# Kernel tuning notes

Hardware: AMD Instinct MI355X
Metric: run time of the kernel (lower is better)

The kernel has to match this reference:

```python
import jax, jax.numpy as jnp
import numpy as np

D = 256
H = 8
FFN = 2048
EPS = 1e-5


def _layer_norm(x, g, b):
    m = jnp.mean(x, axis=-1, keepdims=True)
    v = jnp.mean((x - m) ** 2, axis=-1, keepdims=True)
    return (x - m) * jax.lax.rsqrt(v + EPS) * g + b


def _mha(q_in, k_in, v_in, wq, bq, wk, bk, wv, bv, wo, bo, mask):
    B, Sq, _ = q_in.shape
    Sk = k_in.shape[1]
    dh = D // H
    q = (q_in @ wq + bq).reshape(B, Sq, H, dh)
    k = (k_in @ wk + bk).reshape(B, Sk, H, dh)
    v = (v_in @ wv + bv).reshape(B, Sk, H, dh)
    scores = jnp.einsum('bqhd,bkhd->bhqk', q, k) / jnp.sqrt(jnp.float32(dh)).astype(q.dtype)
    if mask is not None:
        scores = scores + mask
    probs = jax.nn.softmax(scores, axis=-1)
    ctx = jnp.einsum('bhqk,bkhd->bqhd', probs, v).reshape(B, Sq, D)
    return ctx @ wo + bo


def setup_inputs() -> dict:
    key = jax.random.key(0)
    ks = jax.random.split(key, 32)
    s = 0.02
    def lin(i, din, dout):
        return jax.random.normal(ks[i], (din, dout), jnp.float32) * s
    inp = {
        'vision_encoder_hidden_states': jax.random.normal(ks[0], (4, 2048, D), jnp.float32),
        'text_encoder_hidden_states': jax.random.normal(ks[1], (4, 1024, D), jnp.float32),
        'vision_encoder_attention_mask': jnp.zeros((4, 1, 1, 2048), jnp.float32),
        'text_encoder_attention_mask': jnp.zeros((4, 1, 1, 1024), jnp.float32),
        'sa_wq': lin(2, D, D), 'sa_bq': jnp.zeros((D,), jnp.float32),
        'sa_wk': lin(3, D, D), 'sa_bk': jnp.zeros((D,), jnp.float32),
        'sa_wv': lin(4, D, D), 'sa_bv': jnp.zeros((D,), jnp.float32),
        'sa_wo': lin(5, D, D), 'sa_bo': jnp.zeros((D,), jnp.float32),
        'ca_wq': lin(6, D, D), 'ca_bq': jnp.zeros((D,), jnp.float32),
        'ca_wk': lin(7, D, D), 'ca_bk': jnp.zeros((D,), jnp.float32),
        'ca_wv': lin(8, D, D), 'ca_bv': jnp.zeros((D,), jnp.float32),
        'ca_wo': lin(9, D, D), 'ca_bo': jnp.zeros((D,), jnp.float32),
        'ln1_g': jnp.ones((D,), jnp.float32), 'ln1_b': jnp.zeros((D,), jnp.float32),
        'ln2_g': jnp.ones((D,), jnp.float32), 'ln2_b': jnp.zeros((D,), jnp.float32),
        'ln3_g': jnp.ones((D,), jnp.float32), 'ln3_b': jnp.zeros((D,), jnp.float32),
        'ln4_g': jnp.ones((D,), jnp.float32), 'ln4_b': jnp.zeros((D,), jnp.float32),
        'fc1_w': lin(10, D, FFN), 'fc1_b': jnp.zeros((FFN,), jnp.float32),
        'fc2_w': lin(11, FFN, D), 'fc2_b': jnp.zeros((D,), jnp.float32),
    }
    return inp


def reference(vision_encoder_hidden_states, text_encoder_hidden_states,
              vision_encoder_attention_mask, text_encoder_attention_mask,
              sa_wq, sa_bq, sa_wk, sa_bk, sa_wv, sa_bv, sa_wo, sa_bo,
              ca_wq, ca_bq, ca_wk, ca_bk, ca_wv, ca_bv, ca_wo, ca_bo,
              ln1_g, ln1_b, ln2_g, ln2_b, ln3_g, ln3_b, ln4_g, ln4_b,
              fc1_w, fc1_b, fc2_w, fc2_b):
    # self-attention over vision queries (dropout = identity in eval)
    residual = vision_encoder_hidden_states
    h = _mha(vision_encoder_hidden_states, vision_encoder_hidden_states,
             vision_encoder_hidden_states,
             sa_wq, sa_bq, sa_wk, sa_bk, sa_wv, sa_bv, sa_wo, sa_bo,
             vision_encoder_attention_mask)
    h = _layer_norm(residual + h, ln1_g, ln1_b)
    # text cross-attention
    res2 = h
    h = _mha(h, text_encoder_hidden_states, text_encoder_hidden_states,
             ca_wq, ca_bq, ca_wk, ca_bk, ca_wv, ca_bv, ca_wo, ca_bo,
             text_encoder_attention_mask)
    h = _layer_norm(res2 + h, ln2_g, ln2_b)
    # third block: residual + dropout(h) -> in eval this is h + h = 2h, then LN
    h = _layer_norm(h + h, ln3_g, ln3_b)
    # FFN
    res = h
    h = jax.nn.relu(h @ fc1_w + fc1_b)
    h = h @ fc2_w + fc2_b
    h = _layer_norm(res + h, ln4_g, ln4_b)
    return h
```

## Files before the change

### kernel.cpp

```cpp
#include <hip/hip_runtime.h>
#include <stdint.h>
#include <stddef.h>

#define HEADS 8
#define DH 32
#define DMODEL 256
#define LN_EPS 1e-5f
#define LOG2E 1.4426950408889634f
#define QSCALE 0.17677669529663687f
#define QSCALE2 (QSCALE * LOG2E)
#define EXP2(x) __builtin_amdgcn_exp2f(x)

typedef unsigned short u16;
typedef __bf16 bf16x8 __attribute__((ext_vector_type(8)));
typedef unsigned short u16x8 __attribute__((ext_vector_type(8)));
typedef float f32x4 __attribute__((ext_vector_type(4)));

static __device__ __forceinline__ u16 bfc(float f) {
    return __builtin_bit_cast(u16, (__bf16)f);
}
static __device__ __forceinline__ bf16x8 ldbf8(const u16* p) {
    return __builtin_bit_cast(bf16x8, *reinterpret_cast<const u16x8*>(p));
}
static __device__ __forceinline__ bf16x8 cvt8(float4 a, float4 b) {
    bf16x8 r;
    r[0] = (__bf16)a.x; r[1] = (__bf16)a.y; r[2] = (__bf16)a.z; r[3] = (__bf16)a.w;
    r[4] = (__bf16)b.x; r[5] = (__bf16)b.y; r[6] = (__bf16)b.z; r[7] = (__bf16)b.w;
    return r;
}

__global__ __launch_bounds__(256) void scale_mask(const float* __restrict__ in,
                                                  float* __restrict__ out, int n) {
    int i = blockIdx.x * 256 + threadIdx.x;
    if (i < n) out[i] = in[i] * LOG2E;
}

struct TDesc { const float* src; u16* dst; int K; int N; };
struct TArgs { TDesc d[10]; };

__global__ __launch_bounds__(256) void transpose_cvt(TArgs args) {
    TDesc d = args.d[blockIdx.y];
    const int ntx = d.N >> 5;
    const int tiles = (d.K >> 5) * ntx;
    if ((int)blockIdx.x >= tiles) return;
    const int tk = (blockIdx.x / ntx) << 5;
    const int tn = (blockIdx.x % ntx) << 5;
    __shared__ float t[32][33];
    const int lx = threadIdx.x & 31;
    const int ly = threadIdx.x >> 5;
#pragma unroll
    for (int i = 0; i < 4; ++i)
        t[ly + 8 * i][lx] = d.src[(size_t)(tk + ly + 8 * i) * d.N + tn + lx];
    __syncthreads();
#pragma unroll
    for (int i = 0; i < 4; ++i)
        d.dst[(size_t)(tn + ly + 8 * i) * d.K + tk + lx] = bfc(t[lx][ly + 8 * i]);
}

struct Slice { u16* out; const float* bias; int mode; float sc; };

__global__ __launch_bounds__(256) void gemm_xproj(
    const float* __restrict__ Af, const u16* __restrict__ Wt,
    Slice s0, Slice s1, Slice s2, int M, int ntm)
{
    const int lane = threadIdx.x & 63;
    const int wave = threadIdx.x >> 6;
    const int l15 = lane & 15, lhi = lane >> 4;
    const int tm = ((int)blockIdx.x % ntm) * 128;
    const int tn = ((int)blockIdx.x / ntm) * 64;
    const int wm = tm + wave * 32;
    const int sel = tn >> 8;
    const int tl = tn & 255;
    Slice sl = (sel == 0) ? s0 : (sel == 1 ? s1 : s2);

    const f32x4 z4 = {0.f, 0.f, 0.f, 0.f};
    f32x4 acc[2][4];
#pragma unroll
    for (int i = 0; i < 2; ++i)
#pragma unroll
        for (int j = 0; j < 4; ++j) acc[i][j] = z4;

    const float* ar0 = Af + (size_t)(wm + l15) * 256 + lhi * 8;
    const float* ar1 = ar0 + (size_t)16 * 256;
    const u16* b0p = Wt + (size_t)(tn + l15) * 256 + lhi * 8;

    float4 a00 = *(const float4*)(ar0), a01 = *(const float4*)(ar0 + 4);
    float4 a10 = *(const float4*)(ar1), a11 = *(const float4*)(ar1 + 4);
    bf16x8 b[4];
#pragma unroll
    for (int j = 0; j < 4; ++j) b[j] = ldbf8(b0p + (size_t)j * 16 * 256);

#pragma unroll
    for (int k = 32; k < 256; k += 32) {
        float4 n00 = *(const float4*)(ar0 + k), n01 = *(const float4*)(ar0 + k + 4);
        float4 n10 = *(const float4*)(ar1 + k), n11 = *(const float4*)(ar1 + k + 4);
        bf16x8 bn[4];
#pragma unroll
        for (int j = 0; j < 4; ++j) bn[j] = ldbf8(b0p + (size_t)j * 16 * 256 + k);
        bf16x8 a0 = cvt8(a00, a01), a1 = cvt8(a10, a11);
#pragma unroll
        for (int j = 0; j < 4; ++j) {
            acc[0][j] = __builtin_amdgcn_mfma_f32_16x16x32_bf16(a0, b[j], acc[0][j], 0, 0, 0);
            acc[1][j] = __builtin_amdgcn_mfma_f32_16x16x32_bf16(a1, b[j], acc[1][j], 0, 0, 0);
        }
        a00 = n00; a01 = n01; a10 = n10; a11 = n11;
#pragma unroll
        for (int j = 0; j < 4; ++j) b[j] = bn[j];
    }
    {
        bf16x8 a0 = cvt8(a00, a01), a1 = cvt8(a10, a11);
#pragma unroll
        for (int j = 0; j < 4; ++j) {
            acc[0][j] = __builtin_amdgcn_mfma_f32_16x16x32_bf16(a0, b[j], acc[0][j], 0, 0, 0);
            acc[1][j] = __builtin_amdgcn_mfma_f32_16x16x32_bf16(a1, b[j], acc[1][j], 0, 0, 0);
        }
    }

#pragma unroll
    for (int i = 0; i < 2; ++i) {
#pragma unroll
        for (int j = 0; j < 4; ++j) {
            const int col = tl + j * 16 + l15;
            const float bv = sl.bias[col];
            const int row0 = wm + i * 16 + lhi * 4;
            if (sl.mode == 1) {
#pragma unroll
                for (int r = 0; r < 4; ++r)
                    sl.out[(size_t)(row0 + r) * 256 + col] = bfc((acc[i][j][r] + bv) * sl.sc);
            } else {
                ushort4 o = make_ushort4(bfc((acc[i][j][0] + bv) * sl.sc), bfc((acc[i][j][1] + bv) * sl.sc),
                                         bfc((acc[i][j][2] + bv) * sl.sc), bfc((acc[i][j][3] + bv) * sl.sc));
                *reinterpret_cast<ushort4*>(sl.out + (size_t)col * M + row0) = o;
            }
        }
    }
}

template<int MODE, bool RELU>
__global__ __launch_bounds__(256) void gemm_wide(
    const u16* __restrict__ A, const u16* __restrict__ Bt,
    const float* __restrict__ bias, void* __restrict__ Cout,
    int M, int N, int K, int ntm, float osc)
{
    const int lane = threadIdx.x & 63;
    const int wave = threadIdx.x >> 6;
    const int l15 = lane & 15, lhi = lane >> 4;
    const int tm = ((int)blockIdx.x % ntm) * 128;
    const int tn = ((int)blockIdx.x / ntm) * 128;
    const int wm = tm + wave * 32;

    const f32x4 z4 = {0.f, 0.f, 0.f, 0.f};
    f32x4 acc[2][8];
#pragma unroll
    for (int i = 0; i < 2; ++i)
#pragma unroll
        for (int j = 0; j < 8; ++j) acc[i][j] = z4;

    const u16* a0p = A + (size_t)(wm + l15) * K + lhi * 8;
    const u16* a1p = a0p + (size_t)16 * K;
    const u16* b0p = Bt + (size_t)(tn + l15) * K + lhi * 8;

    bf16x8 a0 = ldbf8(a0p), a1 = ldbf8(a1p);
    bf16x8 b[8];
#pragma unroll
    for (int j = 0; j < 8; ++j) b[j] = ldbf8(b0p + (size_t)j * 16 * K);

    for (int k = 32; k < K; k += 32) {
        bf16x8 a0n = ldbf8(a0p + k), a1n = ldbf8(a1p + k);
        bf16x8 bn[8];
#pragma unroll
        for (int j = 0; j < 8; ++j) bn[j] = ldbf8(b0p + (size_t)j * 16 * K + k);
#pragma unroll
        for (int j = 0; j < 8; ++j) {
            acc[0][j] = __builtin_amdgcn_mfma_f32_16x16x32_bf16(a0, b[j], acc[0][j], 0, 0, 0);
            acc[1][j] = __builtin_amdgcn_mfma_f32_16x16x32_bf16(a1, b[j], acc[1][j], 0, 0, 0);
        }
        a0 = a0n; a1 = a1n;
#pragma unroll
        for (int j = 0; j < 8; ++j) b[j] = bn[j];
    }
#pragma unroll
    for (int j = 0; j < 8; ++j) {
        acc[0][j] = __builtin_amdgcn_mfma_f32_16x16x32_bf16(a0, b[j], acc[0][j], 0, 0, 0);
        acc[1][j] = __builtin_amdgcn_mfma_f32_16x16x32_bf16(a1, b[j], acc[1][j], 0, 0, 0);
    }

#pragma unroll
    for (int i = 0; i < 2; ++i) {
#pragma unroll
        for (int j = 0; j < 8; ++j) {
            const int col = tn + j * 16 + l15;
            const float bv = bias[col];
            const int row0 = wm + i * 16 + lhi * 4;
            if (MODE == 0) {
                float* C = (float*)Cout;
#pragma unroll
                for (int r = 0; r < 4; ++r) {
                    float v = acc[i][j][r] + bv;
                    if (RELU) v = fmaxf(v, 0.f);
                    C[(size_t)(row0 + r) * N + col] = v;
                }
            } else {
                u16* C = (u16*)Cout;
#pragma unroll
                for (int r = 0; r < 4; ++r) {
                    float v = acc[i][j][r] + bv;
                    if (RELU) v = fmaxf(v, 0.f);
                    C[(size_t)(row0 + r) * N + col] = bfc(v * osc);
                }
            }
        }
    }
}

__global__ __launch_bounds__(256) void gemm_sk2(
    const u16* __restrict__ A, const u16* __restrict__ Bt,
    const float* __restrict__ bias, float* __restrict__ Cout,
    int M, int N, int lda, int Kh, int ntm)
{
    const int kh = (int)blockIdx.x >= (ntm * (N / 64));
    const int bid = (int)blockIdx.x - kh * (ntm * (N / 64));
    const int lane = threadIdx.x & 63;
    const int wave = threadIdx.x >> 6;
    const int l15 = lane & 15, lhi = lane >> 4;
    const int tm = (bid % ntm) * 128;
    const int tn = (bid / ntm) * 64;
    const int wm = tm + wave * 32;

    const f32x4 z4 = {0.f, 0.f, 0.f, 0.f};
    f32x4 acc[2][4];
#pragma unroll
    for (int i = 0; i < 2; ++i)
#pragma unroll
        for (int j = 0; j < 4; ++j) acc[i][j] = z4;

    const u16* a0p = A + (size_t)(wm + l15) * lda + kh * Kh + lhi * 8;
    const u16* a1p = a0p + (size_t)16 * lda;
    const u16* b0p = Bt + (size_t)(tn + l15) * lda + kh * Kh + lhi * 8;

    bf16x8 a0 = ldbf8(a0p), a1 = ldbf8(a1p);
    bf16x8 b[4];
#pragma unroll
    for (int j = 0; j < 4; ++j) b[j] = ldbf8(b0p + (size_t)j * 16 * lda);

    for (int k = 32; k < Kh; k += 32) {
        bf16x8 a0n = ldbf8(a0p + k), a1n = ldbf8(a1p + k);
        bf16x8 bn[4];
#pragma unroll
        for (int j = 0; j < 4; ++j) bn[j] = ldbf8(b0p + (size_t)j * 16 * lda + k);
#pragma unroll
        for (int j = 0; j < 4; ++j) {
            acc[0][j] = __builtin_amdgcn_mfma_f32_16x16x32_bf16(a0, b[j], acc[0][j], 0, 0, 0);
            acc[1][j] = __builtin_amdgcn_mfma_f32_16x16x32_bf16(a1, b[j], acc[1][j], 0, 0, 0);
        }
        a0 = a0n; a1 = a1n;
#pragma unroll
        for (int j = 0; j < 4; ++j) b[j] = bn[j];
    }
#pragma unroll
    for (int j = 0; j < 4; ++j) {
        acc[0][j] = __builtin_amdgcn_mfma_f32_16x16x32_bf16(a0, b[j], acc[0][j], 0, 0, 0);
        acc[1][j] = __builtin_amdgcn_mfma_f32_16x16x32_bf16(a1, b[j], acc[1][j], 0, 0, 0);
    }

    float* C = Cout + (size_t)kh * M * N;
    const float bs = kh ? 0.f : 1.f;
#pragma unroll
    for (int i = 0; i < 2; ++i) {
#pragma unroll
        for (int j = 0; j < 4; ++j) {
            const int col = tn + j * 16 + l15;
            const float bv = bias[col] * bs;
            const int row0 = wm + i * 16 + lhi * 4;
#pragma unroll
            for (int r = 0; r < 4; ++r)
                C[(size_t)(row0 + r) * N + col] = acc[i][j][r] + bv;
        }
    }
}

template<int MODE, bool RELU>
__global__ __launch_bounds__(256) void gemm64(
    const u16* __restrict__ A, const u16* __restrict__ Bt,
    const float* __restrict__ bias, void* __restrict__ Cout,
    int M, int N, int K, int ntn, float osc)
{
    const int lane = threadIdx.x & 63;
    const int wave = threadIdx.x >> 6;
    const int l15 = lane & 15, lhi = lane >> 4;
    const int tn = ((int)blockIdx.x % ntn) * 64;
    const int tm = ((int)blockIdx.x / ntn) * 64;
    const int wm = tm + (wave & 1) * 32;
    const int wn = tn + (wave >> 1) * 32;

    const f32x4 z4 = {0.f, 0.f, 0.f, 0.f};
    f32x4 acc[2][2] = {{z4, z4}, {z4, z4}};

    const u16* a0p = A + (size_t)(wm + l15) * K + lhi * 8;
    const u16* a1p = a0p + (size_t)16 * K;
    const u16* b0p = Bt + (size_t)(wn + l15) * K + lhi * 8;
    const u16* b1p = b0p + (size_t)16 * K;

    bf16x8 aA0 = ldbf8(a0p), aA1 = ldbf8(a1p), bA0 = ldbf8(b0p), bA1 = ldbf8(b1p);
    bf16x8 aB0 = ldbf8(a0p + 32), aB1 = ldbf8(a1p + 32), bB0 = ldbf8(b0p + 32), bB1 = ldbf8(b1p + 32);

#define G64_MFMA(aX0, aX1, bX0, bX1)                                                        \
    acc[0][0] = __builtin_amdgcn_mfma_f32_16x16x32_bf16(aX0, bX0, acc[0][0], 0, 0, 0);      \
    acc[0][1] = __builtin_amdgcn_mfma_f32_16x16x32_bf16(aX0, bX1, acc[0][1], 0, 0, 0);      \
    acc[1][0] = __builtin_amdgcn_mfma_f32_16x16x32_bf16(aX1, bX0, acc[1][0], 0, 0, 0);      \
    acc[1][1] = __builtin_amdgcn_mfma_f32_16x16x32_bf16(aX1, bX1, acc[1][1], 0, 0, 0);

    for (int k = 64; k < K; k += 64) {
        G64_MFMA(aA0, aA1, bA0, bA1);
        aA0 = ldbf8(a0p + k); aA1 = ldbf8(a1p + k);
        bA0 = ldbf8(b0p + k); bA1 = ldbf8(b1p + k);
        G64_MFMA(aB0, aB1, bB0, bB1);
        aB0 = ldbf8(a0p + k + 32); aB1 = ldbf8(a1p + k + 32);
        bB0 = ldbf8(b0p + k + 32); bB1 = ldbf8(b1p + k + 32);
    }
    G64_MFMA(aA0, aA1, bA0, bA1);
    G64_MFMA(aB0, aB1, bB0, bB1);
#undef G64_MFMA

#pragma unroll
    for (int i = 0; i < 2; ++i) {
#pragma unroll
        for (int j = 0; j < 2; ++j) {
            const int col = wn + j * 16 + l15;
            const float bv = bias[col];
            const int row0 = wm + i * 16 + lhi * 4;
            if (MODE == 0) {
                float* C = (float*)Cout;
#pragma unroll
                for (int r = 0; r < 4; ++r) {
                    float v = acc[i][j][r] + bv;
                    if (RELU) v = fmaxf(v, 0.f);
                    C[(size_t)(row0 + r) * N + col] = v;
                }
            } else {
                u16* C = (u16*)Cout;
#pragma unroll
                for (int r = 0; r < 4; ++r) {
                    float v = acc[i][j][r] + bv;
                    if (RELU) v = fmaxf(v, 0.f);
                    C[(size_t)(row0 + r) * N + col] = bfc(v * osc);
                }
            }
        }
    }
}

__global__ __launch_bounds__(256) void attn_kernel(
    const u16* __restrict__ Qb, const u16* __restrict__ Kb,
    const u16* __restrict__ Vt, const float* __restrict__ mask2,
    u16* __restrict__ Ob, int Sq, int Sk, int MkTot)
{
    const int wave = threadIdx.x >> 6;
    const int lane = threadIdx.x & 63;
    const int l15 = lane & 15, lhi = lane >> 4;
    const int nqc = Sq >> 8;

    const int nwg = (int)gridDim.x;
    const int p = (int)blockIdx.x;
    const int wgid = (p & 7) * (nwg >> 3) + (p >> 3);

    const int bh = wgid / nqc;
    const int qc = wgid % nqc;
    const int b = bh >> 3;
    const int h = bh & 7;
    const int colh = h * DH;
    const int qrow0 = b * Sq + (qc << 8) + wave * 64;
    const int swz = (l15 & 8) << 1;

    __shared__ __align__(16) u16 pt[4][64][72];

    const f32x4 z4 = {0.f, 0.f, 0.f, 0.f};
    const u16 one_bf = 0x3F80;
    u16x8 ones_u;
#pragma unroll
    for (int i = 0; i < 8; ++i) ones_u[i] = one_bf;
    const bf16x8 ones8 = __builtin_bit_cast(bf16x8, ones_u);

    bf16x8 qf[4];
#pragma unroll
    for (int g = 0; g < 4; ++g)
        qf[g] = ldbf8(Qb + (size_t)(qrow0 + g * 16 + l15) * DMODEL + colh + lhi * 8);

    f32x4 ctx[4][2];
    f32x4 ctxS[4];
#pragma unroll
    for (int g = 0; g < 4; ++g) { ctx[g][0] = z4; ctx[g][1] = z4; ctxS[g] = z4; }

    const float* mb = mask2 + (size_t)b * Sk;
    const u16* kbase = Kb + (size_t)(b * Sk) * DMODEL + colh + lhi * 8;
    const u16* vbase = Vt + (size_t)colh * MkTot + (size_t)b * Sk;

    bf16x8 kfA[4], vfA[4], kfB[4], vfB[4];
    f32x4 mcA[4], mcB[4];

#pragma unroll
    for (int j = 0; j < 4; ++j)
        kfA[j] = ldbf8(kbase + (size_t)(j * 16 + l15) * DMODEL);
#pragma unroll
    for (int ks = 0; ks < 2; ++ks)
#pragma unroll
        for (int dt = 0; dt < 2; ++dt)
            vfA[ks * 2 + dt] = ldbf8(vbase + (size_t)(dt * 16 + l15) * MkTot + ks * 32 + lhi * 8);
#pragma unroll
    for (int j = 0; j < 4; ++j)
        mcA[j] = *reinterpret_cast<const f32x4*>(mb + j * 16 + lhi * 4);

#define ATTN_STEP(KC, VC, MC, KN, VN, MN, tpre)                                              \
    {                                                                                        \
        f32x4 s[4][4];                                                                       \
        _Pragma("unroll")                                                                    \
        for (int g = 0; g < 4; ++g)                                                          \
            _Pragma("unroll")                                                                \
            for (int j = 0; j < 4; ++j)                                                      \
                s[g][j] = __builtin_amdgcn_mfma_f32_16x16x32_bf16(KC[j], qf[g], MC[j], 0, 0, 0); \
        const int tp = (tpre);                                                               \
        _Pragma("unroll")                                                                    \
        for (int j = 0; j < 4; ++j)                                                          \
            KN[j] = ldbf8(kbase + (size_t)(tp + j * 16 + l15) * DMODEL);                     \
        _Pragma("unroll")                                                                    \
        for (int ks = 0; ks < 2; ++ks)                                                       \
            _Pragma("unroll")                                                                \
            for (int dt = 0; dt < 2; ++dt)                                                   \
                VN[ks * 2 + dt] = ldbf8(vbase + (size_t)(dt * 16 + l15) * MkTot + tp + ks * 32 + lhi * 8); \
        _Pragma("unroll")                                                                    \
        for (int j = 0; j < 4; ++j)                                                          \
            MN[j] = *reinterpret_cast<const f32x4*>(mb + tp + j * 16 + lhi * 4);             \
        _Pragma("unroll")                                                                    \
        for (int g = 0; g < 4; ++g)                                                          \
            _Pragma("unroll")                                                                \
            for (int j = 0; j < 4; ++j) {                                                    \
                s[g][j][0] = EXP2(s[g][j][0]);                                               \
                s[g][j][1] = EXP2(s[g][j][1]);                                               \
                s[g][j][2] = EXP2(s[g][j][2]);                                               \
                s[g][j][3] = EXP2(s[g][j][3]);                                               \
            }                                                                                \
        asm volatile("" ::: "memory");                                                       \
        _Pragma("unroll")                                                                    \
        for (int g = 0; g < 4; ++g)                                                          \
            _Pragma("unroll")                                                                \
            for (int j = 0; j < 4; ++j) {                                                    \
                ushort4 w = make_ushort4(bfc(s[g][j][0]), bfc(s[g][j][1]),                   \
                                         bfc(s[g][j][2]), bfc(s[g][j][3]));                  \
                *reinterpret_cast<ushort4*>(&pt[wave][g * 16 + l15][(j * 16 + lhi * 4) ^ swz]) = w; \
            }                                                                                \
        asm volatile("" ::: "memory");                                                       \
        _Pragma("unroll")                                                                    \
        for (int ks = 0; ks < 2; ++ks) {                                                     \
            bf16x8 pa[4];                                                                    \
            _Pragma("unroll")                                                                \
            for (int g = 0; g < 4; ++g)                                                      \
                pa[g] = ldbf8(&pt[wave][g * 16 + l15][(ks * 32 + lhi * 8) ^ swz]);           \
            _Pragma("unroll")                                                                \
            for (int g = 0; g < 4; ++g) {                                                    \
                _Pragma("unroll")                                                            \
                for (int dt = 0; dt < 2; ++dt)                                               \
                    ctx[g][dt] = __builtin_amdgcn_mfma_f32_16x16x32_bf16(pa[g], VC[ks * 2 + dt], ctx[g][dt], 0, 0, 0); \
                ctxS[g] = __builtin_amdgcn_mfma_f32_16x16x32_bf16(pa[g], ones8, ctxS[g], 0, 0, 0); \
            }                                                                                \
        }                                                                                    \
    }

    const int NT = Sk >> 6;
    for (int t = 0; t < NT; t += 2) {
        const int t1 = (t + 1) << 6;
        ATTN_STEP(kfA, vfA, mcA, kfB, vfB, mcB, t1);
        const int t2 = ((t + 2 < NT) ? t + 2 : t + 1) << 6;
        ATTN_STEP(kfB, vfB, mcB, kfA, vfA, mcA, t2);
    }
#undef ATTN_STEP

#pragma unroll
    for (int g = 0; g < 4; ++g)
#pragma unroll
        for (int r = 0; r < 4; ++r) {
            const float inv = 1.0f / ctxS[g][r];
            const int row = qrow0 + g * 16 + lhi * 4 + r;
#pragma unroll
            for (int dt = 0; dt < 2; ++dt)
                Ob[(size_t)row * DMODEL + colh + dt * 16 + l15] = bfc(ctx[g][dt][r] * inv);
        }
}

template<bool DBL, bool WBF, bool SPLIT>
__global__ __launch_bounds__(256) void ln_kernel(
    const float* __restrict__ X, const float* __restrict__ X2, const float* __restrict__ Res,
    const float* __restrict__ g1p, const float* __restrict__ b1p,
    const float* __restrict__ g2p, const float* __restrict__ b2p,
    float* __restrict__ Of, u16* __restrict__ Oh)
{
    const int lane = threadIdx.x & 63;
    const int row = blockIdx.x * 4 + (threadIdx.x >> 6);
    const size_t base = (size_t)row * DMODEL + lane * 4;
    float4 x = *reinterpret_cast<const float4*>(X + base);
    float4 rr = *reinterpret_cast<const float4*>(Res + base);
    float v[4] = {x.x + rr.x, x.y + rr.y, x.z + rr.z, x.w + rr.w};
    if constexpr (SPLIT) {
        float4 x2 = *reinterpret_cast<const float4*>(X2 + base);
        v[0] += x2.x; v[1] += x2.y; v[2] += x2.z; v[3] += x2.w;
    }
    float s = v[0] + v[1] + v[2] + v[3];
    float q = v[0] * v[0] + v[1] * v[1] + v[2] * v[2] + v[3] * v[3];
#pragma unroll
    for (int m = 1; m < 64; m <<= 1) { s += __shfl_xor(s, m, 64); q += __shfl_xor(q, m, 64); }
    float mean = s * (1.0f / DMODEL);
    float rstd = rsqrtf(fmaxf(q * (1.0f / DMODEL) - mean * mean, 0.f) + LN_EPS);
    float4 g = *reinterpret_cast<const float4*>(g1p + lane * 4);
    float4 bb = *reinterpret_cast<const float4*>(b1p + lane * 4);
    float y[4];
    y[0] = (v[0] - mean) * rstd * g.x + bb.x;
    y[1] = (v[1] - mean) * rstd * g.y + bb.y;
    y[2] = (v[2] - mean) * rstd * g.z + bb.z;
    y[3] = (v[3] - mean) * rstd * g.w + bb.w;
    if constexpr (DBL) {
#pragma unroll
        for (int k2 = 0; k2 < 4; ++k2) y[k2] *= 2.0f;
        float s2 = y[0] + y[1] + y[2] + y[3];
        float q2 = y[0] * y[0] + y[1] * y[1] + y[2] * y[2] + y[3] * y[3];
#pragma unroll
        for (int m = 1; m < 64; m <<= 1) { s2 += __shfl_xor(s2, m, 64); q2 += __shfl_xor(q2, m, 64); }
        float mean2 = s2 * (1.0f / DMODEL);
        float rstd2 = rsqrtf(fmaxf(q2 * (1.0f / DMODEL) - mean2 * mean2, 0.f) + LN_EPS);
        float4 g2 = *reinterpret_cast<const float4*>(g2p + lane * 4);
        float4 b2 = *reinterpret_cast<const float4*>(b2p + lane * 4);
        y[0] = (y[0] - mean2) * rstd2 * g2.x + b2.x;
        y[1] = (y[1] - mean2) * rstd2 * g2.y + b2.y;
        y[2] = (y[2] - mean2) * rstd2 * g2.z + b2.z;
        y[3] = (y[3] - mean2) * rstd2 * g2.w + b2.w;
    }
    *reinterpret_cast<float4*>(Of + base) = make_float4(y[0], y[1], y[2], y[3]);
    if constexpr (WBF) {
        ushort4 o = make_ushort4(bfc(y[0]), bfc(y[1]), bfc(y[2]), bfc(y[3]));
        *reinterpret_cast<ushort4*>(Oh + base) = o;
    }
}

extern "C" void kernel_launch(void* const* d_in, const int* in_sizes, int n_in,
                              void* d_out, int out_size, void* d_ws, size_t ws_size,
                              hipStream_t stream) {
    constexpr size_t MB = 1u << 20;
    if (ws_size < 70 * MB) return;

    const float* vis   = (const float*)d_in[0];
    const float* txt   = (const float*)d_in[1];
    const float* vmask = (const float*)d_in[2];
    const float* tmask = (const float*)d_in[3];
    const float* sa_wq = (const float*)d_in[4];  const float* sa_bq = (const float*)d_in[5];
    const float* sa_wk = (const float*)d_in[6];  const float* sa_bk = (const float*)d_in[7];
    const float* sa_wv = (const float*)d_in[8];  const float* sa_bv = (const float*)d_in[9];
    const float* sa_wo = (const float*)d_in[10]; const float* sa_bo = (const float*)d_in[11];
    const float* ca_wq = (const float*)d_in[12]; const float* ca_bq = (const float*)d_in[13];
    const float* ca_wk = (const float*)d_in[14]; const float* ca_bk = (const float*)d_in[15];
    const float* ca_wv = (const float*)d_in[16]; const float* ca_bv = (const float*)d_in[17];
    const float* ca_wo = (const float*)d_in[18]; const float* ca_bo = (const float*)d_in[19];
    const float* ln1_g = (const float*)d_in[20]; const float* ln1_b = (const float*)d_in[21];
    const float* ln2_g = (const float*)d_in[22]; const float* ln2_b = (const float*)d_in[23];
    const float* ln3_g = (const float*)d_in[24]; const float* ln3_b = (const float*)d_in[25];
    const float* ln4_g = (const float*)d_in[26]; const float* ln4_b = (const float*)d_in[27];
    const float* fc1_w = (const float*)d_in[28]; const float* fc1_b = (const float*)d_in[29];
    const float* fc2_w = (const float*)d_in[30]; const float* fc2_b = (const float*)d_in[31];

    const int B = 4, Sq = 2048, St = 1024;
    const int Mq = B * Sq;
    const int Mt = B * St;

    char* ws = (char*)d_ws;
    u16*   q_bf    = (u16*)(ws + 6 * MB);
    u16*   k_bf    = (u16*)(ws + 10 * MB);
    u16*   vt_bf   = (u16*)(ws + 14 * MB);
    u16*   ctx_bf  = (u16*)(ws + 18 * MB);
    u16*   ffn1_bf = (u16*)(ws + 0);
    float* attn_f  = (float*)(ws + 32 * MB);
    float* h1_f    = (float*)(ws + 40 * MB);
    u16*   h1_bf   = (u16*)(ws + 48 * MB);
    float* h3_f    = (float*)(ws + 52 * MB);
    u16*   h3_bf   = (u16*)(ws + 60 * MB);
    u16*   wts     = (u16*)(ws + 64 * MB);
    float* ffn2a   = attn_f;
    float* ffn2b   = h1_f;

    u16* wqkv_t = wts;
    u16* wkv_t  = wqkv_t + 768 * 256;
    u16* cwq_t  = wkv_t + 512 * 256;
    u16* wo_t   = cwq_t + 65536;
    u16* cwo_t  = wo_t + 65536;
    u16* fc1_t  = cwo_t + 65536;
    u16* fc2_t  = fc1_t + 2048 * 256;
    float* vmask2 = (float*)(ws + 68 * MB);
    float* tmask2 = vmask2 + B * Sq;

    scale_mask<<<dim3((B * Sq + 255) / 256), 256, 0, stream>>>(vmask, vmask2, B * Sq);
    scale_mask<<<dim3((B * St + 255) / 256), 256, 0, stream>>>(tmask, tmask2, B * St);

    TArgs ta;
    ta.d[0] = {sa_wq, wqkv_t + 0 * 65536, 256, 256};
    ta.d[1] = {sa_wk, wqkv_t + 1 * 65536, 256, 256};
    ta.d[2] = {sa_wv, wqkv_t + 2 * 65536, 256, 256};
    ta.d[3] = {ca_wk, wkv_t + 0 * 65536, 256, 256};
    ta.d[4] = {ca_wv, wkv_t + 1 * 65536, 256, 256};
    ta.d[5] = {ca_wq, cwq_t, 256, 256};
    ta.d[6] = {sa_wo, wo_t, 256, 256};
    ta.d[7] = {ca_wo, cwo_t, 256, 256};
    ta.d[8] = {fc1_w, fc1_t, 256, 2048};
    ta.d[9] = {fc2_w, fc2_t, 2048, 256};
    transpose_cvt<<<dim3(512, 10), 256, 0, stream>>>(ta);

    Slice sq = {q_bf, sa_bq, 1, QSCALE2}, sk = {k_bf, sa_bk, 1, 1.f}, sv = {vt_bf, sa_bv, 2, 1.f};
    gemm_xproj<<<dim3((Mq / 128) * 12), 256, 0, stream>>>(vis, wqkv_t, sq, sk, sv, Mq, Mq / 128);
    attn_kernel<<<dim3(B * HEADS * (Sq / 256)), 256, 0, stream>>>(q_bf, k_bf, vt_bf, vmask2, ctx_bf, Sq, Sq, Mq);
    gemm64<0, false><<<dim3((Mq / 64) * 4), 256, 0, stream>>>(ctx_bf, wo_t, sa_bo, attn_f, Mq, 256, 256, 4, 1.f);
    ln_kernel<false, true, false><<<dim3(Mq / 4), 256, 0, stream>>>(attn_f, nullptr, vis, ln1_g, ln1_b, nullptr, nullptr, h1_f, h1_bf);

    Slice ck = {k_bf, ca_bk, 1, 1.f}, cv = {vt_bf, ca_bv, 2, 1.f}, cd = {nullptr, nullptr, 1, 1.f};
    gemm_xproj<<<dim3((Mt / 128) * 8), 256, 0, stream>>>(txt, wkv_t, ck, cv, cd, Mt, Mt / 128);
    gemm64<1, false><<<dim3((Mq / 64) * 4), 256, 0, stream>>>(h1_bf, cwq_t, ca_bq, q_bf, Mq, 256, 256, 4, QSCALE2);
    attn_kernel<<<dim3(B * HEADS * (Sq / 256)), 256, 0, stream>>>(q_bf, k_bf, vt_bf, tmask2, ctx_bf, Sq, St, Mt);
    gemm64<0, false><<<dim3((Mq / 64) * 4), 256, 0, stream>>>(ctx_bf, cwo_t, ca_bo, attn_f, Mq, 256, 256, 4, 1.f);
    ln_kernel<true, true, false><<<dim3(Mq / 4), 256, 0, stream>>>(attn_f, nullptr, h1_f, ln2_g, ln2_b, ln3_g, ln3_b, h3_f, h3_bf);

    gemm_wide<1, true><<<dim3((Mq / 128) * 16), 256, 0, stream>>>(h3_bf, fc1_t, fc1_b, ffn1_bf, Mq, 2048, 256, Mq / 128, 1.f);
    gemm_sk2<<<dim3((Mq / 128) * 4 * 2), 256, 0, stream>>>(ffn1_bf, fc2_t, fc2_b, ffn2a, Mq, 256, 2048, 1024, Mq / 128);
    ln_kernel<false, false, true><<<dim3(Mq / 4), 256, 0, stream>>>(ffn2a, ffn2b, h3_f, ln4_g, ln4_b, nullptr, nullptr, (float*)d_out, nullptr);
}
```

Before: 246.8 us.

## Shrink FC2 split-K tile to 64x64 with 2x2 wave layout and deeper prefetch

The split-K FC2 GEMM now uses 64x64 output tiles, with four waves arranged 2x2 at 32x32 each, instead of 128x64 tiles. This doubles the grid to 1024 blocks so more CUs are busy. The K loop is unrolled by two, with double-buffered register loads covering 64 K-elements ahead. The trade-off is less A/B reuse per block, so more redundant global loads for fewer accumulators per wave.

```diff
diff --git a/kernel.cpp b/kernel.cpp
--- a/kernel.cpp
+++ b/kernel.cpp
@@ -218,58 +218,53 @@
     const float* __restrict__ bias, float* __restrict__ Cout,
     int M, int N, int lda, int Kh, int ntm)
 {
-    const int kh = (int)blockIdx.x >= (ntm * (N / 64));
-    const int bid = (int)blockIdx.x - kh * (ntm * (N / 64));
+    const int half = ntm * (N / 64);
+    const int kh = (int)blockIdx.x >= half;
+    const int bid = (int)blockIdx.x - kh * half;
     const int lane = threadIdx.x & 63;
     const int wave = threadIdx.x >> 6;
     const int l15 = lane & 15, lhi = lane >> 4;
-    const int tm = (bid % ntm) * 128;
+    const int tm = (bid % ntm) * 64;
     const int tn = (bid / ntm) * 64;
-    const int wm = tm + wave * 32;
+    const int wm = tm + (wave & 1) * 32;
+    const int wn = tn + (wave >> 1) * 32;
 
     const f32x4 z4 = {0.f, 0.f, 0.f, 0.f};
-    f32x4 acc[2][4];
-#pragma unroll
-    for (int i = 0; i < 2; ++i)
-#pragma unroll
-        for (int j = 0; j < 4; ++j) acc[i][j] = z4;
+    f32x4 acc[2][2] = {{z4, z4}, {z4, z4}};
 
     const u16* a0p = A + (size_t)(wm + l15) * lda + kh * Kh + lhi * 8;
     const u16* a1p = a0p + (size_t)16 * lda;
-    const u16* b0p = Bt + (size_t)(tn + l15) * lda + kh * Kh + lhi * 8;
-
-    bf16x8 a0 = ldbf8(a0p), a1 = ldbf8(a1p);
-    bf16x8 b[4];
-#pragma unroll
-    for (int j = 0; j < 4; ++j) b[j] = ldbf8(b0p + (size_t)j * 16 * lda);
-
-    for (int k = 32; k < Kh; k += 32) {
-        bf16x8 a0n = ldbf8(a0p + k), a1n = ldbf8(a1p + k);
-        bf16x8 bn[4];
-#pragma unroll
-        for (int j = 0; j < 4; ++j) bn[j] = ldbf8(b0p + (size_t)j * 16 * lda + k);
-#pragma unroll
-        for (int j = 0; j < 4; ++j) {
-            acc[0][j] = __builtin_amdgcn_mfma_f32_16x16x32_bf16(a0, b[j], acc[0][j], 0, 0, 0);
-            acc[1][j] = __builtin_amdgcn_mfma_f32_16x16x32_bf16(a1, b[j], acc[1][j], 0, 0, 0);
-        }
-        a0 = a0n; a1 = a1n;
-#pragma unroll
-        for (int j = 0; j < 4; ++j) b[j] = bn[j];
-    }
-#pragma unroll
-    for (int j = 0; j < 4; ++j) {
-        acc[0][j] = __builtin_amdgcn_mfma_f32_16x16x32_bf16(a0, b[j], acc[0][j], 0, 0, 0);
-        acc[1][j] = __builtin_amdgcn_mfma_f32_16x16x32_bf16(a1, b[j], acc[1][j], 0, 0, 0);
-    }
+    const u16* b0p = Bt + (size_t)(wn + l15) * lda + kh * Kh + lhi * 8;
+    const u16* b1p = b0p + (size_t)16 * lda;
+
+    bf16x8 aA0 = ldbf8(a0p), aA1 = ldbf8(a1p), bA0 = ldbf8(b0p), bA1 = ldbf8(b1p);
+    bf16x8 aB0 = ldbf8(a0p + 32), aB1 = ldbf8(a1p + 32), bB0 = ldbf8(b0p + 32), bB1 = ldbf8(b1p + 32);
+
+#define SK2_MFMA(aX0, aX1, bX0, bX1)                                                        \
+    acc[0][0] = __builtin_amdgcn_mfma_f32_16x16x32_bf16(aX0, bX0, acc[0][0], 0, 0, 0);      \
+    acc[0][1] = __builtin_amdgcn_mfma_f32_16x16x32_bf16(aX0, bX1, acc[0][1], 0, 0, 0);      \
+    acc[1][0] = __builtin_amdgcn_mfma_f32_16x16x32_bf16(aX1, bX0, acc[1][0], 0, 0, 0);      \
+    acc[1][1] = __builtin_amdgcn_mfma_f32_16x16x32_bf16(aX1, bX1, acc[1][1], 0, 0, 0);
+
+    for (int k = 64; k < Kh; k += 64) {
+        SK2_MFMA(aA0, aA1, bA0, bA1);
+        aA0 = ldbf8(a0p + k); aA1 = ldbf8(a1p + k);
+        bA0 = ldbf8(b0p + k); bA1 = ldbf8(b1p + k);
+        SK2_MFMA(aB0, aB1, bB0, bB1);
+        aB0 = ldbf8(a0p + k + 32); aB1 = ldbf8(a1p + k + 32);
+        bB0 = ldbf8(b0p + k + 32); bB1 = ldbf8(b1p + k + 32);
+    }
+    SK2_MFMA(aA0, aA1, bA0, bA1);
+    SK2_MFMA(aB0, aB1, bB0, bB1);
+#undef SK2_MFMA
 
     float* C = Cout + (size_t)kh * M * N;
     const float bs = kh ? 0.f : 1.f;
 #pragma unroll
     for (int i = 0; i < 2; ++i) {
 #pragma unroll
-        for (int j = 0; j < 4; ++j) {
-            const int col = tn + j * 16 + l15;
+        for (int j = 0; j < 2; ++j) {
+            const int col = wn + j * 16 + l15;
             const float bv = bias[col] * bs;
             const int row0 = wm + i * 16 + lhi * 4;
 #pragma unroll
@@ -623,6 +618,6 @@
     ln_kernel<true, true, false><<<dim3(Mq / 4), 256, 0, stream>>>(attn_f, nullptr, h1_f, ln2_g, ln2_b, ln3_g, ln3_b, h3_f, h3_bf);
 
     gemm_wide<1, true><<<dim3((Mq / 128) * 16), 256, 0, stream>>>(h3_bf, fc1_t, fc1_b, ffn1_bf, Mq, 2048, 256, Mq / 128, 1.f);
-    gemm_sk2<<<dim3((Mq / 128) * 4 * 2), 256, 0, stream>>>(ffn1_bf, fc2_t, fc2_b, ffn2a, Mq, 256, 2048, 1024, Mq / 128);
+    gemm_sk2<<<dim3((Mq / 64) * 4 * 2), 256, 0, stream>>>(ffn1_bf, fc2_t, fc2_b, ffn2a, Mq, 256, 2048, 1024, Mq / 64);
     ln_kernel<false, false, true><<<dim3(Mq / 4), 256, 0, stream>>>(ffn2a, ffn2b, h3_f, ln4_g, ln4_b, nullptr, nullptr, (float*)d_out, nullptr);
 }
```

New measurement: 259.4 us. 5.1% more time.
